# Performance work log

Hardware: AMD Instinct MI355X
Metric: run time of the kernel (lower is better)

Reference implementation:

```python
import math
import jax, jax.numpy as jnp
import numpy as np

D_MODEL, N_HEADS, QKV, D_HEAD, D_FF, N_BLOCKS, IN_DIM = 288, 8, 328, 41, 1315, 4, 83
B, S = 1024, 128
EPS = 1e-5


def setup_inputs() -> dict:
    key = jax.random.key(0)
    ks = iter(jax.random.split(key, 64))
    def rn(shape, scale=0.05):
        return jax.random.normal(next(ks), shape, jnp.float32) * scale
    inp = {
        "x": jax.random.normal(next(ks), (B, S, IN_DIM), jnp.float32),
        "Wp": rn((D_MODEL, IN_DIM)), "bp": rn((D_MODEL,)),
        "phase": rn((D_MODEL,)),
        "Wq": rn((N_BLOCKS, QKV, D_MODEL)), "bq": rn((N_BLOCKS, QKV)),
        "Wk": rn((N_BLOCKS, QKV, D_MODEL)), "bk": rn((N_BLOCKS, QKV)),
        "Wv": rn((N_BLOCKS, QKV, D_MODEL)), "bv": rn((N_BLOCKS, QKV)),
        "Wo": rn((N_BLOCKS, D_MODEL, QKV)), "bo": rn((N_BLOCKS, D_MODEL)),
        "temp": jnp.ones((N_BLOCKS,), jnp.float32) + rn((N_BLOCKS,), 0.01),
        "qscale": jnp.ones((N_BLOCKS, N_HEADS), jnp.float32) + rn((N_BLOCKS, N_HEADS), 0.01),
        "Wf1": rn((N_BLOCKS, D_FF, D_MODEL)), "bf1": rn((N_BLOCKS, D_FF)),
        "Wf2": rn((N_BLOCKS, D_MODEL, D_FF)), "bf2": rn((N_BLOCKS, D_MODEL)),
        "n1w": jnp.ones((N_BLOCKS, D_MODEL), jnp.float32), "n1b": jnp.zeros((N_BLOCKS, D_MODEL), jnp.float32),
        "n2w": jnp.ones((N_BLOCKS, D_MODEL), jnp.float32), "n2b": jnp.zeros((N_BLOCKS, D_MODEL), jnp.float32),
        "skip": jnp.ones((N_BLOCKS,), jnp.float32),
        "bn_w": jnp.ones((D_MODEL,), jnp.float32), "bn_b": jnp.zeros((D_MODEL,), jnp.float32),
        "bn_mean": rn((D_MODEL,)), "bn_var": jax.random.uniform(next(ks), (D_MODEL,), jnp.float32, 0.5, 1.5),
        "h1w": rn((144, D_MODEL)), "h1b": rn((144,)),
        "h2w": rn((72, 144)), "h2b": rn((72,)),
        "h3w": rn((1, 72)), "h3b": rn((1,)),
        "u1w": rn((72, D_MODEL)), "u1b": rn((72,)),
        "u2w": rn((1, 72)), "u2b": rn((1,)),
    }
    return inp


def _layer_norm(x, w, b):
    mu = jnp.mean(x, axis=-1, keepdims=True)
    var = jnp.mean((x - mu) ** 2, axis=-1, keepdims=True)
    return (x - mu) * jax.lax.rsqrt(var + EPS) * w + b


def reference(x, Wp, bp, phase, Wq, bq, Wk, bk, Wv, bv, Wo, bo, temp, qscale,
              Wf1, bf1, Wf2, bf2, n1w, n1b, n2w, n2b, skip,
              bn_w, bn_b, bn_mean, bn_var,
              h1w, h1b, h2w, h2b, h3w, h3b, u1w, u1b, u2w, u2b):
    Bsz, Sl, _ = x.shape
    # input projection
    h = jnp.einsum('bsi,di->bsd', x, Wp) + bp
    # sinusoidal positional encoding modulated by cos(quantum_phase)
    pos = jnp.arange(Sl, dtype=jnp.float32)[:, None]
    div = jnp.exp(jnp.arange(0, D_MODEL, 2, dtype=jnp.float32) * (-math.log(10000.0) / D_MODEL))
    pe = jnp.zeros((Sl, D_MODEL), jnp.float32)
    pe = pe.at[:, 0::2].set(jnp.sin(pos * div)).at[:, 1::2].set(jnp.cos(pos * div))
    h = h + pe * jnp.cos(phase)

    for l in range(N_BLOCKS):
        # attention with temperature-scaled softmax + post-softmax per-head scale
        q = (jnp.einsum('bsd,qd->bsq', h, Wq[l]) + bq[l]).reshape(Bsz, Sl, N_HEADS, D_HEAD)
        k = (jnp.einsum('bsd,qd->bsq', h, Wk[l]) + bk[l]).reshape(Bsz, Sl, N_HEADS, D_HEAD)
        v = (jnp.einsum('bsd,qd->bsq', h, Wv[l]) + bv[l]).reshape(Bsz, Sl, N_HEADS, D_HEAD)
        scale = math.sqrt(D_HEAD) * temp[l]
        scores = jnp.einsum('bqhd,bkhd->bhqk', q, k) / scale  # [B,H,S,S]
        attn = jax.nn.softmax(scores, axis=-1) * qscale[l][None, :, None, None]
        o = jnp.einsum('bhqk,bkhd->bqhd', attn, v).reshape(Bsz, Sl, QKV)
        o = jnp.einsum('bsq,dq->bsd', o, Wo[l]) + bo[l]
        h = _layer_norm(h + skip[l] * o, n1w[l], n1b[l])
        # GELU FFN (exact erf gelu, dropout inactive in eval)
        f = jax.nn.gelu(jnp.einsum('bsd,fd->bsf', h, Wf1[l]) + bf1[l], approximate=False)
        f = jnp.einsum('bsf,df->bsd', f, Wf2[l]) + bf2[l]
        h = _layer_norm(h + f, n2w[l], n2b[l])

    pooled = jnp.mean(h, axis=1)  # [B, D_MODEL]
    # output head: BatchNorm1d (eval, running stats) -> GELU -> MLP
    z = (pooled - bn_mean) * jax.lax.rsqrt(bn_var + EPS) * bn_w + bn_b
    z = jax.nn.gelu(z, approximate=False)
    z = jax.nn.gelu(z @ h1w.T + h1b, approximate=False)
    z = jax.nn.gelu(z @ h2w.T + h2b, approximate=False)
    pred = z @ h3w.T + h3b  # [B, 1]
    # uncertainty head
    u = jax.nn.relu(pooled @ u1w.T + u1b)
    unc = jax.nn.softplus(u @ u2w.T + u2b)  # [B, 1]
    return pred, unc
```

## Files before the change

### kernel.cpp

```cpp
#include <hip/hip_runtime.h>
#include <cstdint>

typedef __attribute__((ext_vector_type(8))) short short8;
typedef __attribute__((ext_vector_type(4))) short s4v;
typedef __attribute__((ext_vector_type(4))) float floatx4;

#define DEV __device__ __forceinline__

DEV short f2bf(float f) {
  unsigned u = __builtin_bit_cast(unsigned, f);
  u += 0x7fffu + ((u >> 16) & 1u);
  return (short)(u >> 16);
}
DEV short f2bf_ru(float f) {
  unsigned u = __builtin_bit_cast(unsigned, f);
  return (short)((u + 0x8000u) >> 16);
}
DEV float bf2f(short s) {
  unsigned u = ((unsigned)(unsigned short)s) << 16;
  return __builtin_bit_cast(float, u);
}
DEV float gelu_exact(float x) {
  return 0.5f * x * (1.0f + erff(x * 0.70710678118654752f));
}
DEV float gelu_fast(float x) {
  const float t2 = 1.5957691216057308f * (x + 0.044715f * x * x * x);
  return x / (1.0f + __expf(-t2));
}
DEV void gload16(const void* g, void* l) {
  __builtin_amdgcn_global_load_lds((const __attribute__((address_space(1))) void*)g,
                                   (__attribute__((address_space(3))) void*)l,
                                   16, 0, 0);
}

template<int MODE>
__global__ __launch_bounds__(256)
void gemm_kernel(const short* __restrict__ A, const short* __restrict__ Bw,
                 const float* __restrict__ bias, short* __restrict__ C,
                 const float* __restrict__ pe,
                 int K, int lda, int ldb, int ldc, int Nstore, int NT, long hstride)
{
  __shared__ __align__(16) short lds[128 * 136];
  short* As = lds;
  short* Bs = lds + 128 * 32;
  short* Ct = lds;

  const int tid  = threadIdx.x;
  const int wave = tid >> 6, lane = tid & 63;
  const int quad = lane >> 4, r16 = lane & 15;
  const int per = gridDim.x >> 3;
  const int gti = (blockIdx.x & 7) * per + (blockIdx.x >> 3);
  const int mt = gti / NT, nt = gti - mt * NT;
  const int wm = (wave >> 1) * 64, wn = (wave & 1) * 64;

  const long Abase = (long)mt * 128 * lda;
  const long Bbase = (long)nt * 128 * ldb;

  const int row0 = tid >> 2,         cc0 = (tid & 3) ^ ((row0 >> 1) & 3);
  const int row1 = (256 + tid) >> 2, cc1 = ((256 + tid) & 3) ^ ((row1 >> 1) & 3);

  floatx4 acc[4][4] = {};

  for (int k0 = 0; k0 < K; k0 += 32) {
    __syncthreads();
    gload16(A  + Abase + (long)row0 * lda + k0 + cc0 * 8, &As[(0 * 256 + wave * 64) * 8]);
    gload16(A  + Abase + (long)row1 * lda + k0 + cc1 * 8, &As[(1 * 256 + wave * 64) * 8]);
    gload16(Bw + Bbase + (long)row0 * ldb + k0 + cc0 * 8, &Bs[(0 * 256 + wave * 64) * 8]);
    gload16(Bw + Bbase + (long)row1 * ldb + k0 + cc1 * 8, &Bs[(1 * 256 + wave * 64) * 8]);
    __syncthreads();

    short8 af[4], bfr[4];
#pragma unroll
    for (int i = 0; i < 4; ++i) {
      const int R = wm + i * 16 + r16;
      af[i] = *(const short8*)&As[R * 32 + (quad ^ ((R >> 1) & 3)) * 8];
    }
#pragma unroll
    for (int j = 0; j < 4; ++j) {
      const int R = wn + j * 16 + r16;
      bfr[j] = *(const short8*)&Bs[R * 32 + (quad ^ ((R >> 1) & 3)) * 8];
    }
#pragma unroll
    for (int i = 0; i < 4; ++i)
#pragma unroll
      for (int j = 0; j < 4; ++j)
        acc[i][j] = __builtin_amdgcn_mfma_f32_16x16x32_bf16(bfr[j], af[i], acc[i][j], 0, 0, 0);
  }

  const int mb0 = mt * 128, tb = nt * 128;

  __syncthreads();
#pragma unroll
  for (int j = 0; j < 4; ++j) {
    const int n0 = wn + j * 16 + quad * 4;
    const floatx4 b4 = *(const floatx4*)&bias[tb + n0];
#pragma unroll
    for (int i = 0; i < 4; ++i) {
      const int m = wm + i * 16 + r16;
      floatx4 v = acc[i][j] + b4;
      if (MODE == 1) {
#pragma unroll
        for (int rg = 0; rg < 4; ++rg) v[rg] = gelu_fast(v[rg]);
      }
      if (MODE == 2) {
        const floatx4 p4 = *(const floatx4*)&pe[((mb0 + m) & 127) * 384 + tb + n0];
        v = v + p4;
      }
      s4v o4;
#pragma unroll
      for (int rg = 0; rg < 4; ++rg) o4[rg] = f2bf_ru(v[rg]);
      *(s4v*)&Ct[m * 136 + n0] = o4;
    }
  }
  __syncthreads();

#pragma unroll
  for (int rr = 0; rr < 8; ++rr) {
    const int chunk = rr * 256 + tid;
    const int row = chunk >> 4, ch = chunk & 15;
    const int gcol = tb + ch * 8;
    if (MODE == 3) {
      const int g = gcol / 48, d0 = gcol - g * 48;
      *(short8*)(C + (long)g * hstride + (long)(mb0 + row) * 48 + d0) =
          *(const short8*)&Ct[row * 136 + ch * 8];
    } else if (gcol < Nstore) {
      *(short8*)(C + (long)(mb0 + row) * ldc + gcol) = *(const short8*)&Ct[row * 136 + ch * 8];
    }
  }
}

template<bool AHEAD>
__global__ __launch_bounds__(512, 4)
void gemm_ln_kernel(const short* __restrict__ A, const short* __restrict__ Bw,
                    const float* __restrict__ bias, short* __restrict__ h,
                    const float* __restrict__ lnw, const float* __restrict__ lnb,
                    const float* __restrict__ skip_p, int layer, int use_skip,
                    int K, int lda, int ldb, long ahs)
{
  __shared__ __align__(16) short lds[128 * 296];
  short* As = lds;
  short* Bs = lds + 128 * 32;
  short* Hs = lds;

  const int tid  = threadIdx.x;
  const int wave = tid >> 6, lane = tid & 63;
  const int quad = lane >> 4, r16 = lane & 15;
  const int mt = blockIdx.x;
  const long mrow0 = (long)mt * 128;

  floatx4 acc[18] = {};

  for (int k0 = 0; k0 < K; k0 += 32) {
    __syncthreads();
    for (int c = tid; c < 1664; c += 512) {
      const void* src;
      if (c < 512) {
        const int row = c >> 2, cc = (c & 3) ^ ((row >> 1) & 3);
        if (AHEAD) {
          const int kc = k0 + cc * 8;
          const int g = kc / 48, d = kc - g * 48;
          src = A + (long)g * ahs + (mrow0 + row) * 48 + d;
        } else {
          src = A + (mrow0 + row) * lda + k0 + cc * 8;
        }
      } else {
        const int cb = c - 512;
        const int row = cb >> 2, cc = (cb & 3) ^ ((row >> 1) & 3);
        src = Bw + (long)row * ldb + k0 + cc * 8;
      }
      gload16(src, &lds[(size_t)(c & ~63) * 8]);
    }
    __syncthreads();

    const int Ra = wave * 16 + r16;
    const short8 af = *(const short8*)&As[Ra * 32 + (quad ^ ((Ra >> 1) & 3)) * 8];
#pragma unroll
    for (int t = 0; t < 18; ++t) {
      const int Rb = t * 16 + r16;
      const short8 bfr = *(const short8*)&Bs[Rb * 32 + (quad ^ ((Rb >> 1) & 3)) * 8];
      acc[t] = __builtin_amdgcn_mfma_f32_16x16x32_bf16(bfr, af, acc[t], 0, 0, 0);
    }
  }

  __syncthreads();
  for (int c = tid; c < 4608; c += 512) {
    const int row = c / 36, ch = c - row * 36;
    *(short8*)&Hs[row * 296 + ch * 8] =
        *(const short8*)(h + (mrow0 + row) * 288 + ch * 8);
  }
  __syncthreads();

  const float skipv = use_skip ? skip_p[layer] : 1.0f;
  const int m = wave * 16 + r16;

  float ps = 0.f, pss = 0.f;
#pragma unroll
  for (int t = 0; t < 18; ++t) {
    const int n0 = t * 16 + quad * 4;
    const floatx4 b4 = *(const floatx4*)&bias[n0];
    const s4v h4 = *(const s4v*)&Hs[m * 296 + n0];
#pragma unroll
    for (int rg = 0; rg < 4; ++rg) {
      const float y = bf2f(h4[rg]) + skipv * (acc[t][rg] + b4[rg]);
      acc[t][rg] = y;
      ps += y; pss += y * y;
    }
  }
  ps  += __shfl_xor(ps, 16);  ps  += __shfl_xor(ps, 32);
  pss += __shfl_xor(pss, 16); pss += __shfl_xor(pss, 32);
  const float mean = ps * (1.f / 288.f);
  const float var  = pss * (1.f / 288.f) - mean * mean;
  const float rstd = rsqrtf(var + 1e-5f);

#pragma unroll
  for (int t = 0; t < 18; ++t) {
    const int n0 = t * 16 + quad * 4;
    const floatx4 w4 = *(const floatx4*)&lnw[n0];
    const floatx4 l4 = *(const floatx4*)&lnb[n0];
    s4v o4;
#pragma unroll
    for (int rg = 0; rg < 4; ++rg)
      o4[rg] = f2bf_ru((acc[t][rg] - mean) * rstd * w4[rg] + l4[rg]);
    *(s4v*)&Hs[m * 296 + n0] = o4;
  }
  __syncthreads();

  for (int c = tid; c < 4608; c += 512) {
    const int row = c / 36, ch = c - row * 36;
    *(short8*)(h + (mrow0 + row) * 288 + ch * 8) =
        *(const short8*)&Hs[row * 296 + ch * 8];
  }
}

__global__ __launch_bounds__(256)
void attn_kernel(short* __restrict__ qkv,
                 const float* __restrict__ qscale, int layer, long Mc)
{
  __shared__ __align__(16) short qk[2 * 128 * 72];
  __shared__ __align__(16) short vsT[48 * 136 + 32];
  __shared__ float red[2][2][64];

  short* qs = qk;
  short* ks = qk + 128 * 72;
  short* Pb = qk;

  const int b = blockIdx.x, h = blockIdx.y;
  const int tid = threadIdx.x;
  const long sec = Mc * 48;
  const short* qg = qkv + (long)h * sec + (long)b * 128 * 48;
  const short* kg = qg + 8 * sec;
  const short* vg = qg + 16 * sec;
  short* og = qkv + (long)(16 + h) * sec + (long)b * 128 * 48;

  for (int c = tid; c < 768; c += 256) {
    const int s = c / 6, dc = c - (c / 6) * 6;
    *(short8*)&qs[s * 72 + dc * 8] = *(const short8*)(qg + (long)s * 48 + dc * 8);
    *(short8*)&ks[s * 72 + dc * 8] = *(const short8*)(kg + (long)s * 48 + dc * 8);
  }
  {
    short8 z;
#pragma unroll
    for (int j = 0; j < 8; ++j) z[j] = 0;
    for (int c = tid; c < 384; c += 256) {
      const int s = c / 3, t = c - (c / 3) * 3;
      *(short8*)&qs[s * 72 + 48 + t * 8] = z;
      *(short8*)&ks[s * 72 + 48 + t * 8] = z;
    }
  }
  for (int c = tid; c < 768; c += 256) {
    const int s = c & 127, dc = c >> 7;
    const short8 tv = *(const short8*)(vg + (long)s * 48 + dc * 8);
#pragma unroll
    for (int j = 0; j < 8; ++j) {
      const int row = dc * 8 + j;
      vsT[row * 136 + ((row >> 3) & 3) * 8 + s] = tv[j];
    }
  }
  __syncthreads();

  const int wave = tid >> 6, lane = tid & 63;
  const int quad = lane >> 4, r16 = lane & 15;
  const int wm = (wave >> 1) * 64, wn = (wave & 1) * 64;
  const int rh = wave >> 1, ch = wave & 1;
  const float qsc = qscale[layer * 8 + h];

  floatx4 acc[4][4] = {};
#pragma unroll
  for (int kk = 0; kk < 2; ++kk) {
    const int k0 = kk * 32;
    short8 af[4], bfr[4];
#pragma unroll
    for (int i = 0; i < 4; ++i)
      af[i] = *(const short8*)&qs[(wm + i * 16 + r16) * 72 + k0 + quad * 8];
#pragma unroll
    for (int j = 0; j < 4; ++j)
      bfr[j] = *(const short8*)&ks[(wn + j * 16 + r16) * 72 + k0 + quad * 8];
#pragma unroll
    for (int i = 0; i < 4; ++i)
#pragma unroll
      for (int j = 0; j < 4; ++j)
        acc[i][j] = __builtin_amdgcn_mfma_f32_16x16x32_bf16(bfr[j], af[i], acc[i][j], 0, 0, 0);
  }

  float rmax[4], rsum[4];
#pragma unroll
  for (int i = 0; i < 4; ++i) {
    float m = acc[i][0][0];
#pragma unroll
    for (int j = 0; j < 4; ++j)
#pragma unroll
      for (int rg = 0; rg < 4; ++rg) m = fmaxf(m, acc[i][j][rg]);
    m = fmaxf(m, __shfl_xor(m, 16));
    m = fmaxf(m, __shfl_xor(m, 32));
    rmax[i] = m;
  }
  if (lane < 16)
#pragma unroll
    for (int i = 0; i < 4; ++i) red[rh][ch][i * 16 + r16] = rmax[i];
  __syncthreads();
#pragma unroll
  for (int i = 0; i < 4; ++i)
    rmax[i] = fmaxf(red[rh][0][i * 16 + r16], red[rh][1][i * 16 + r16]);

#pragma unroll
  for (int i = 0; i < 4; ++i) {
    float s = 0.f;
#pragma unroll
    for (int j = 0; j < 4; ++j)
#pragma unroll
      for (int rg = 0; rg < 4; ++rg) {
        const float e = __expf(acc[i][j][rg] - rmax[i]);
        acc[i][j][rg] = e;
        s += e;
      }
    s += __shfl_xor(s, 16);
    s += __shfl_xor(s, 32);
    rsum[i] = s;
  }
  __syncthreads();
  if (lane < 16)
#pragma unroll
    for (int i = 0; i < 4; ++i) red[rh][ch][i * 16 + r16] = rsum[i];
  __syncthreads();
#pragma unroll
  for (int i = 0; i < 4; ++i)
    rmax[i] = qsc / (red[rh][0][i * 16 + r16] + red[rh][1][i * 16 + r16]);

#pragma unroll
  for (int i = 0; i < 4; ++i) {
    const int sq = wm + i * 16 + r16;
#pragma unroll
    for (int j = 0; j < 4; ++j) {
      const int sk0 = wn + j * 16 + quad * 4;
      s4v p4;
#pragma unroll
      for (int rg = 0; rg < 4; ++rg) p4[rg] = f2bf_ru(acc[i][j][rg] * rmax[i]);
      *(s4v*)&Pb[sq * 136 + sk0] = p4;
    }
  }
  __syncthreads();

  const int om = (wave >> 1) * 64, on = (wave & 1) * 32;
  const int jn = (on == 0) ? 2 : 1;
  floatx4 oacc[4][2] = {};
  for (int kk = 0; kk < 4; ++kk) {
    const int k0 = kk * 32;
    short8 af[4], bfr[2];
#pragma unroll
    for (int i = 0; i < 4; ++i)
      af[i] = *(const short8*)&Pb[(om + i * 16 + r16) * 136 + k0 + quad * 8];
    for (int j = 0; j < jn; ++j) {
      const int row = on + j * 16 + r16;
      bfr[j] = *(const short8*)&vsT[row * 136 + ((row >> 3) & 3) * 8 + k0 + quad * 8];
    }
#pragma unroll
    for (int i = 0; i < 4; ++i)
      for (int j = 0; j < jn; ++j)
        oacc[i][j] = __builtin_amdgcn_mfma_f32_16x16x32_bf16(bfr[j], af[i], oacc[i][j], 0, 0, 0);
  }
#pragma unroll
  for (int i = 0; i < 4; ++i)
    for (int j = 0; j < jn; ++j) {
      const int d0 = on + j * 16 + quad * 4;
      const int sq = om + i * 16 + r16;
      s4v o4;
#pragma unroll
      for (int rg = 0; rg < 4; ++rg) o4[rg] = f2bf_ru(oacc[i][j][rg]);
      *(s4v*)(og + (long)sq * 48 + d0) = o4;
    }
}

__global__ __launch_bounds__(256)
void head_kernel(const short* __restrict__ hb, float* __restrict__ out,
                 const float* bn_w, const float* bn_b, const float* bn_mean, const float* bn_var,
                 const float* h1w, const float* h1b, const float* h2w, const float* h2b,
                 const float* h3w, const float* h3b,
                 const float* u1w, const float* u1b, const float* u2w, const float* u2b)
{
  __shared__ float psum[252][8];
  __shared__ float pooled[288], z[288], z1[144], z2[72], uu[72];
  const int b = blockIdx.x, tid = threadIdx.x;

  if (tid < 252) {
    const int cch = tid % 36, grp = tid / 36;
    float a[8];
#pragma unroll
    for (int j = 0; j < 8; ++j) a[j] = 0.f;
    for (int r = grp; r < 128; r += 7) {
      const short8 hv = *(const short8*)(hb + ((long)b * 128 + r) * 288 + cch * 8);
#pragma unroll
      for (int j = 0; j < 8; ++j) a[j] += bf2f(hv[j]);
    }
#pragma unroll
    for (int j = 0; j < 8; ++j) psum[tid][j] = a[j];
  }
  __syncthreads();
  for (int d = tid; d < 288; d += 256) {
    const int cch = d >> 3, j = d & 7;
    float s = 0.f;
#pragma unroll
    for (int g = 0; g < 7; ++g) s += psum[g * 36 + cch][j];
    pooled[d] = s * (1.f / 128.f);
  }
  __syncthreads();

  for (int d = tid; d < 288; d += 256) {
    const float p = pooled[d];
    z[d] = gelu_exact((p - bn_mean[d]) * rsqrtf(bn_var[d] + 1e-5f) * bn_w[d] + bn_b[d]);
  }
  __syncthreads();

  if (tid < 144) {
    float s = h1b[tid];
    for (int k = 0; k < 288; ++k) s += z[k] * h1w[tid * 288 + k];
    z1[tid] = gelu_exact(s);
  } else if (tid < 216) {
    const int t = tid - 144;
    float s = u1b[t];
    for (int k = 0; k < 288; ++k) s += pooled[k] * u1w[t * 288 + k];
    uu[t] = fmaxf(s, 0.f);
  }
  __syncthreads();

  if (tid < 72) {
    float s = h2b[tid];
    for (int k = 0; k < 144; ++k) s += z1[k] * h2w[tid * 144 + k];
    z2[tid] = gelu_exact(s);
  }
  __syncthreads();

  if (tid == 0) {
    float s = h3b[0];
    for (int k = 0; k < 72; ++k) s += z2[k] * h3w[k];
    out[b] = s;
  }
  if (tid == 64) {
    float s = u2b[0];
    for (int k = 0; k < 72; ++k) s += uu[k] * u2w[k];
    out[1024 + b] = (s > 20.f) ? s : log1pf(__expf(s));
  }
}

__global__ void conv_w_kernel(const float* __restrict__ src, short* __restrict__ dst,
                              int N, int K, int Npad, int Kpad, int total)
{
  const int i = blockIdx.x * 256 + threadIdx.x;
  if (i >= total) return;
  const int kk = i % Kpad;
  const int t  = i / Kpad;
  const int n  = t % Npad;
  const int l  = t / Npad;
  const float v = (n < N && kk < K) ? src[((long)l * N + n) * K + kk] : 0.f;
  dst[i] = f2bf(v);
}

__global__ void conv_b_kernel(const float* __restrict__ src, float* __restrict__ dst,
                              int N, int Npad, int total)
{
  const int i = blockIdx.x * 256 + threadIdx.x;
  if (i >= total) return;
  const int n = i % Npad, l = i / Npad;
  dst[i] = (n < N) ? src[l * N + n] : 0.f;
}

__global__ void conv_wqkv_kernel(const float* __restrict__ Wq, const float* __restrict__ Wk,
                                 const float* __restrict__ Wv, const float* __restrict__ temp,
                                 short* __restrict__ dst)
{
  const int i = blockIdx.x * 256 + threadIdx.x;
  if (i >= 4 * 1152 * 288) return;
  const int kk = i % 288;
  const int t  = i / 288;
  const int r  = t % 1152;
  const int l  = t / 1152;
  const int g  = r / 48, d = r - (r / 48) * 48;
  const int sec = g >> 3, head = g & 7;
  float v = 0.f;
  if (d < 41) {
    const float* W = (sec == 0) ? Wq : (sec == 1) ? Wk : Wv;
    v = W[((long)l * 328 + head * 41 + d) * 288 + kk];
    if (sec == 0) v *= 1.0f / (6.4031242374328485f * temp[l]);
  }
  dst[i] = f2bf(v);
}

__global__ void conv_bqkv_kernel(const float* __restrict__ bq, const float* __restrict__ bk,
                                 const float* __restrict__ bv, const float* __restrict__ temp,
                                 float* __restrict__ dst)
{
  const int i = blockIdx.x * 256 + threadIdx.x;
  if (i >= 4 * 1152) return;
  const int r = i % 1152, l = i / 1152;
  const int g = r / 48, d = r - (r / 48) * 48;
  const int sec = g >> 3, head = g & 7;
  float v = 0.f;
  if (d < 41) {
    const float* b = (sec == 0) ? bq : (sec == 1) ? bk : bv;
    v = b[l * 328 + head * 41 + d];
    if (sec == 0) v *= 1.0f / (6.4031242374328485f * temp[l]);
  }
  dst[i] = v;
}

__global__ void conv_wo_kernel(const float* __restrict__ Wo, short* __restrict__ dst)
{
  const int i = blockIdx.x * 256 + threadIdx.x;
  if (i >= 4 * 288 * 384) return;
  const int kk = i % 384;
  const int t  = i / 384;
  const int n  = t % 288;
  const int l  = t / 288;
  const int head = kk / 48, d = kk - head * 48;
  float v = 0.f;
  if (d < 41) v = Wo[((long)l * 288 + n) * 328 + head * 41 + d];
  dst[i] = f2bf(v);
}

__global__ void conv_x_kernel(const float* __restrict__ x, short* __restrict__ xb, int total)
{
  const int i = blockIdx.x * 256 + threadIdx.x;
  if (i >= total) return;
  const int c = i % 96;
  const int r = i / 96;
  xb[i] = f2bf((c < 83) ? x[(long)r * 83 + c] : 0.f);
}

__global__ void pe_kernel(const float* __restrict__ phase, float* __restrict__ pe_mod)
{
  const int i = blockIdx.x * 256 + threadIdx.x;
  if (i >= 128 * 384) return;
  const int d = i % 384, s = i / 384;
  float out = 0.f;
  if (d < 288) {
    const int pair = d >> 1;
    const float divv = expf((float)(2 * pair) * (-9.210340371976184f / 288.f));
    const float arg = (float)s * divv;
    const float v = (d & 1) ? cosf(arg) : sinf(arg);
    out = v * cosf(phase[d]);
  }
  pe_mod[i] = out;
}

extern "C" void kernel_launch(void* const* d_in, const int* in_sizes, int n_in,
                              void* d_out, int out_size, void* d_ws, size_t ws_size,
                              hipStream_t stream)
{
  (void)in_sizes; (void)n_in; (void)out_size;

  const float* x     = (const float*)d_in[0];
  const float* Wp    = (const float*)d_in[1];
  const float* bp    = (const float*)d_in[2];
  const float* phase = (const float*)d_in[3];
  const float* Wq    = (const float*)d_in[4];
  const float* bq    = (const float*)d_in[5];
  const float* Wk    = (const float*)d_in[6];
  const float* bk    = (const float*)d_in[7];
  const float* Wv    = (const float*)d_in[8];
  const float* bv    = (const float*)d_in[9];
  const float* Wo    = (const float*)d_in[10];
  const float* bo    = (const float*)d_in[11];
  const float* temp  = (const float*)d_in[12];
  const float* qscale= (const float*)d_in[13];
  const float* Wf1   = (const float*)d_in[14];
  const float* bf1   = (const float*)d_in[15];
  const float* Wf2   = (const float*)d_in[16];
  const float* bf2   = (const float*)d_in[17];
  const float* n1w   = (const float*)d_in[18];
  const float* n1b   = (const float*)d_in[19];
  const float* n2w   = (const float*)d_in[20];
  const float* n2b   = (const float*)d_in[21];
  const float* skip  = (const float*)d_in[22];
  const float* bn_w  = (const float*)d_in[23];
  const float* bn_b  = (const float*)d_in[24];
  const float* bn_mean=(const float*)d_in[25];
  const float* bn_var= (const float*)d_in[26];
  const float* h1w   = (const float*)d_in[27];
  const float* h1b   = (const float*)d_in[28];
  const float* h2w   = (const float*)d_in[29];
  const float* h2b   = (const float*)d_in[30];
  const float* h3w   = (const float*)d_in[31];
  const float* h3b   = (const float*)d_in[32];
  const float* u1w   = (const float*)d_in[33];
  const float* u1b   = (const float*)d_in[34];
  const float* u2w   = (const float*)d_in[35];
  const float* u2b   = (const float*)d_in[36];

  char* ws = (char*)d_ws;
  size_t off = 0;
  auto alloc = [&](size_t n) -> char* {
    off = (off + 255) & ~(size_t)255;
    char* p = ws + off;
    off += n;
    return p;
  };

  const long M = 131072;

  short* h_bf   = (short*)alloc((size_t)M * 288 * 2);
  float* pe_mod = (float*)alloc(128 * 384 * 4);

  short* Wp_b   = (short*)alloc((size_t)384 * 96 * 2);
  short* Wqkv_b = (short*)alloc((size_t)4 * 1152 * 288 * 2);
  short* Wo_b   = (short*)alloc((size_t)4 * 288 * 384 * 2);
  short* Wf1_b  = (short*)alloc((size_t)4 * 1408 * 288 * 2);
  short* Wf2_b  = (short*)alloc((size_t)4 * 384 * 1344 * 2);

  float* bp_p   = (float*)alloc((size_t)384 * 4);
  float* bqkv_p = (float*)alloc((size_t)4 * 1152 * 4);
  float* bo_p   = (float*)alloc((size_t)4 * 384 * 4);
  float* bf1_p  = (float*)alloc((size_t)4 * 1408 * 4);
  float* bf2_p  = (float*)alloc((size_t)4 * 384 * 4);

  const size_t fixed = off;
  int NC = 1;
  while (NC < 16 && fixed + (size_t)(M / NC) * 2304 + (1u << 20) > ws_size) NC <<= 1;
  const long Mc = M / NC;
  const long Mc2 = Mc / 2;
  const long sec = Mc * 48;

  char* R = alloc((size_t)Mc * 2304);
  short* qkv_bf = (short*)R;
  short* f_bf   = (short*)R;
  short* x_bfc  = (short*)R;

  const dim3 blk(256);

  auto conv_w = [&](const float* s, short* d, int N, int K, int Np, int Kp, int L) {
    const int total = L * Np * Kp;
    conv_w_kernel<<<dim3((total + 255) / 256), blk, 0, stream>>>(s, d, N, K, Np, Kp, total);
  };
  auto conv_b = [&](const float* s, float* d, int N, int Np, int L) {
    const int total = L * Np;
    conv_b_kernel<<<dim3((total + 255) / 256), blk, 0, stream>>>(s, d, N, Np, total);
  };
  conv_w(Wp,  Wp_b,  288,   83, 384,   96, 1);
  conv_wqkv_kernel<<<dim3((4 * 1152 * 288 + 255) / 256), blk, 0, stream>>>(Wq, Wk, Wv, temp, Wqkv_b);
  conv_wo_kernel<<<dim3((4 * 288 * 384 + 255) / 256), blk, 0, stream>>>(Wo, Wo_b);
  conv_w(Wf1, Wf1_b, 1315, 288, 1408, 288, 4);
  conv_w(Wf2, Wf2_b, 288, 1315, 384, 1344, 4);
  conv_b(bp,  bp_p,  288,  384, 1);
  conv_bqkv_kernel<<<dim3((4 * 1152 + 255) / 256), blk, 0, stream>>>(bq, bk, bv, temp, bqkv_p);
  conv_b(bo,  bo_p,  288,  384, 4);
  conv_b(bf1, bf1_p, 1315, 1408, 4);
  conv_b(bf2, bf2_p, 288,  384, 4);
  pe_kernel<<<dim3((128 * 384 + 255) / 256), blk, 0, stream>>>(phase, pe_mod);

  auto gemm = [&](int mode, const short* A, const short* Bmat, const float* bias,
                  short* C, const float* pe, int K, int lda, int ldb, int ldc,
                  int Nstore, int NT, long Mrows, long hstride) {
    const dim3 grid((unsigned)((Mrows / 128) * NT));
    switch (mode) {
      case 0: gemm_kernel<0><<<grid, blk, 0, stream>>>(A, Bmat, bias, C, pe, K, lda, ldb, ldc, Nstore, NT, hstride); break;
      case 1: gemm_kernel<1><<<grid, blk, 0, stream>>>(A, Bmat, bias, C, pe, K, lda, ldb, ldc, Nstore, NT, hstride); break;
      case 2: gemm_kernel<2><<<grid, blk, 0, stream>>>(A, Bmat, bias, C, pe, K, lda, ldb, ldc, Nstore, NT, hstride); break;
      default: gemm_kernel<3><<<grid, blk, 0, stream>>>(A, Bmat, bias, C, pe, K, lda, ldb, ldc, Nstore, NT, hstride); break;
    }
  };

  for (int c = 0; c < NC; ++c) {
    const float* x_c = x + (size_t)c * Mc * 83;
    short* h_c = h_bf + (size_t)c * Mc * 288;

    const int xtot = (int)(Mc * 96);
    conv_x_kernel<<<dim3((xtot + 255) / 256), blk, 0, stream>>>(x_c, x_bfc, xtot);

    gemm(2, x_bfc, Wp_b, bp_p, h_c, pe_mod, 96, 96, 96, 288, 288, 3, Mc, 0);

    for (int l = 0; l < 4; ++l) {
      const short* Wqkv_l = Wqkv_b + (size_t)l * 1152 * 288;
      const short* Wo_l   = Wo_b   + (size_t)l * 288 * 384;
      const short* Wf1_l  = Wf1_b  + (size_t)l * 1408 * 288;
      const short* Wf2_l  = Wf2_b  + (size_t)l * 384 * 1344;

      gemm(3, h_c, Wqkv_l, bqkv_p + l * 1152, qkv_bf, nullptr,
           288, 288, 288, 0, 1152, 9, Mc, sec);

      attn_kernel<<<dim3((unsigned)(Mc / 128), 8), blk, 0, stream>>>(
          qkv_bf, qscale, l, Mc);

      gemm_ln_kernel<true><<<dim3((unsigned)(Mc / 128)), dim3(512), 0, stream>>>(
          qkv_bf + 16 * sec, Wo_l, bo_p + l * 384, h_c, n1w + l * 288, n1b + l * 288,
          skip, l, 1, 384, 48, 384, sec);

      for (int s = 0; s < 2; ++s) {
        short* h_s = h_c + (size_t)s * Mc2 * 288;
        gemm(1, h_s, Wf1_l, bf1_p + l * 1408, f_bf, nullptr,
             288, 288, 288, 1344, 1344, 11, Mc2, 0);
        gemm_ln_kernel<false><<<dim3((unsigned)(Mc2 / 128)), dim3(512), 0, stream>>>(
            f_bf, Wf2_l, bf2_p + l * 384, h_s, n2w + l * 288, n2b + l * 288,
            skip, l, 0, 1344, 1344, 1344, 0);
      }
    }
  }

  head_kernel<<<dim3(1024), blk, 0, stream>>>(h_bf, (float*)d_out,
      bn_w, bn_b, bn_mean, bn_var,
      h1w, h1b, h2w, h2b, h3w, h3b,
      u1w, u1b, u2w, u2b);
}
```

Baseline: 3.710 ms.

## Double-buffer LDS staging in GEMM kernels and retile GEMM+LayerNorm waves to 2x2

Both the plain GEMM and the fused GEMM+LayerNorm kernels now use two LDS buffers, issuing global-to-LDS loads for the next K slice before computing on the current one, with one barrier per iteration instead of two. The GEMM+LN kernel also changes its wave layout from 8x1 (16 rows by all 288 cols) to 4x2 (32 rows by 144 cols), so each B fragment feeds two MFMAs. Row statistics are then combined across the two column waves through a small shared-memory reduction with an extra barrier. The intent is to hide load latency and cut LDS B-fragment reads, at the cost of more LDS use (which may limit occupancy) and the extra reduction step.

```diff
diff --git a/kernel.cpp b/kernel.cpp
--- a/kernel.cpp
+++ b/kernel.cpp
@@ -41,8 +41,6 @@
                  int K, int lda, int ldb, int ldc, int Nstore, int NT, long hstride)
 {
   __shared__ __align__(16) short lds[128 * 136];
-  short* As = lds;
-  short* Bs = lds + 128 * 32;
   short* Ct = lds;
 
   const int tid  = threadIdx.x;
@@ -61,35 +59,54 @@
 
   floatx4 acc[4][4] = {};
 
-  for (int k0 = 0; k0 < K; k0 += 32) {
-    __syncthreads();
-    gload16(A  + Abase + (long)row0 * lda + k0 + cc0 * 8, &As[(0 * 256 + wave * 64) * 8]);
-    gload16(A  + Abase + (long)row1 * lda + k0 + cc1 * 8, &As[(1 * 256 + wave * 64) * 8]);
-    gload16(Bw + Bbase + (long)row0 * ldb + k0 + cc0 * 8, &Bs[(0 * 256 + wave * 64) * 8]);
-    gload16(Bw + Bbase + (long)row1 * ldb + k0 + cc1 * 8, &Bs[(1 * 256 + wave * 64) * 8]);
-    __syncthreads();
-
+  auto stage = [&](short* As_, short* Bs_, int k0) {
+    gload16(A  + Abase + (long)row0 * lda + k0 + cc0 * 8, &As_[(wave * 64) * 8]);
+    gload16(A  + Abase + (long)row1 * lda + k0 + cc1 * 8, &As_[(256 + wave * 64) * 8]);
+    gload16(Bw + Bbase + (long)row0 * ldb + k0 + cc0 * 8, &Bs_[(wave * 64) * 8]);
+    gload16(Bw + Bbase + (long)row1 * ldb + k0 + cc1 * 8, &Bs_[(256 + wave * 64) * 8]);
+  };
+  auto compute = [&](const short* As_, const short* Bs_) {
     short8 af[4], bfr[4];
 #pragma unroll
     for (int i = 0; i < 4; ++i) {
       const int R = wm + i * 16 + r16;
-      af[i] = *(const short8*)&As[R * 32 + (quad ^ ((R >> 1) & 3)) * 8];
+      af[i] = *(const short8*)&As_[R * 32 + (quad ^ ((R >> 1) & 3)) * 8];
     }
 #pragma unroll
     for (int j = 0; j < 4; ++j) {
       const int R = wn + j * 16 + r16;
-      bfr[j] = *(const short8*)&Bs[R * 32 + (quad ^ ((R >> 1) & 3)) * 8];
+      bfr[j] = *(const short8*)&Bs_[R * 32 + (quad ^ ((R >> 1) & 3)) * 8];
     }
 #pragma unroll
     for (int i = 0; i < 4; ++i)
 #pragma unroll
       for (int j = 0; j < 4; ++j)
         acc[i][j] = __builtin_amdgcn_mfma_f32_16x16x32_bf16(bfr[j], af[i], acc[i][j], 0, 0, 0);
+  };
+
+  short* const A0  = lds;
+  short* const Bb0 = lds + 4096;
+  short* const A1  = lds + 8192;
+  short* const Bb1 = lds + 12288;
+
+  stage(A0, Bb0, 0);
+  __syncthreads();
+  int k0 = 0;
+  while (true) {
+    if (k0 + 32 < K) stage(A1, Bb1, k0 + 32);
+    compute(A0, Bb0);
+    __syncthreads();
+    k0 += 32;
+    if (k0 >= K) break;
+    if (k0 + 32 < K) stage(A0, Bb0, k0 + 32);
+    compute(A1, Bb1);
+    __syncthreads();
+    k0 += 32;
+    if (k0 >= K) break;
   }
 
   const int mb0 = mt * 128, tb = nt * 128;
 
-  __syncthreads();
 #pragma unroll
   for (int j = 0; j < 4; ++j) {
     const int n0 = wn + j * 16 + quad * 4;
@@ -138,20 +155,20 @@
                     int K, int lda, int ldb, long ahs)
 {
   __shared__ __align__(16) short lds[128 * 296];
-  short* As = lds;
-  short* Bs = lds + 128 * 32;
+  __shared__ float redp[4][2][2][16];
+  __shared__ float reds[4][2][2][16];
   short* Hs = lds;
 
   const int tid  = threadIdx.x;
   const int wave = tid >> 6, lane = tid & 63;
   const int quad = lane >> 4, r16 = lane & 15;
+  const int wr = wave >> 1, wc = wave & 1;
   const int mt = blockIdx.x;
   const long mrow0 = (long)mt * 128;
 
-  floatx4 acc[18] = {};
-
-  for (int k0 = 0; k0 < K; k0 += 32) {
-    __syncthreads();
+  floatx4 acc[2][9] = {};
+
+  auto stage = [&](short* buf, int k0) {
     for (int c = tid; c < 1664; c += 512) {
       const void* src;
       if (c < 512) {
@@ -168,21 +185,44 @@
         const int row = cb >> 2, cc = (cb & 3) ^ ((row >> 1) & 3);
         src = Bw + (long)row * ldb + k0 + cc * 8;
       }
-      gload16(src, &lds[(size_t)(c & ~63) * 8]);
-    }
+      gload16(src, &buf[(size_t)(c & ~63) * 8]);
+    }
+  };
+
+  auto compute = [&](const short* buf) {
+    const short* As_ = buf;
+    const short* Bs_ = buf + 4096;
+    const int Ra0 = wr * 32 + r16, Ra1 = Ra0 + 16;
+    const short8 af0 = *(const short8*)&As_[Ra0 * 32 + (quad ^ ((Ra0 >> 1) & 3)) * 8];
+    const short8 af1 = *(const short8*)&As_[Ra1 * 32 + (quad ^ ((Ra1 >> 1) & 3)) * 8];
+#pragma unroll
+    for (int t = 0; t < 9; ++t) {
+      const int Rb = wc * 144 + t * 16 + r16;
+      const short8 b = *(const short8*)&Bs_[Rb * 32 + (quad ^ ((Rb >> 1) & 3)) * 8];
+      acc[0][t] = __builtin_amdgcn_mfma_f32_16x16x32_bf16(b, af0, acc[0][t], 0, 0, 0);
+      acc[1][t] = __builtin_amdgcn_mfma_f32_16x16x32_bf16(b, af1, acc[1][t], 0, 0, 0);
+    }
+  };
+
+  short* const B0 = lds;
+  short* const B1 = lds + 13312;
+
+  stage(B0, 0);
+  __syncthreads();
+  int k0 = 0;
+  while (true) {
+    if (k0 + 32 < K) stage(B1, k0 + 32);
+    compute(B0);
     __syncthreads();
-
-    const int Ra = wave * 16 + r16;
-    const short8 af = *(const short8*)&As[Ra * 32 + (quad ^ ((Ra >> 1) & 3)) * 8];
-#pragma unroll
-    for (int t = 0; t < 18; ++t) {
-      const int Rb = t * 16 + r16;
-      const short8 bfr = *(const short8*)&Bs[Rb * 32 + (quad ^ ((Rb >> 1) & 3)) * 8];
-      acc[t] = __builtin_amdgcn_mfma_f32_16x16x32_bf16(bfr, af, acc[t], 0, 0, 0);
-    }
-  }
-
-  __syncthreads();
+    k0 += 32;
+    if (k0 >= K) break;
+    if (k0 + 32 < K) stage(B0, k0 + 32);
+    compute(B1);
+    __syncthreads();
+    k0 += 32;
+    if (k0 >= K) break;
+  }
+
   for (int c = tid; c < 4608; c += 512) {
     const int row = c / 36, ch = c - row * 36;
     *(short8*)&Hs[row * 296 + ch * 8] =
@@ -191,37 +231,54 @@
   __syncthreads();
 
   const float skipv = use_skip ? skip_p[layer] : 1.0f;
-  const int m = wave * 16 + r16;
-
-  float ps = 0.f, pss = 0.f;
-#pragma unroll
-  for (int t = 0; t < 18; ++t) {
-    const int n0 = t * 16 + quad * 4;
+  const int m0 = wr * 32 + r16, m1 = m0 + 16;
+
+  float ps0 = 0.f, ss0 = 0.f, ps1 = 0.f, ss1 = 0.f;
+#pragma unroll
+  for (int t = 0; t < 9; ++t) {
+    const int n0 = wc * 144 + t * 16 + quad * 4;
     const floatx4 b4 = *(const floatx4*)&bias[n0];
-    const s4v h4 = *(const s4v*)&Hs[m * 296 + n0];
+    const s4v h40 = *(const s4v*)&Hs[m0 * 296 + n0];
+    const s4v h41 = *(const s4v*)&Hs[m1 * 296 + n0];
 #pragma unroll
     for (int rg = 0; rg < 4; ++rg) {
-      const float y = bf2f(h4[rg]) + skipv * (acc[t][rg] + b4[rg]);
-      acc[t][rg] = y;
-      ps += y; pss += y * y;
-    }
-  }
-  ps  += __shfl_xor(ps, 16);  ps  += __shfl_xor(ps, 32);
-  pss += __shfl_xor(pss, 16); pss += __shfl_xor(pss, 32);
-  const float mean = ps * (1.f / 288.f);
-  const float var  = pss * (1.f / 288.f) - mean * mean;
-  const float rstd = rsqrtf(var + 1e-5f);
-
-#pragma unroll
-  for (int t = 0; t < 18; ++t) {
-    const int n0 = t * 16 + quad * 4;
+      const float y0 = bf2f(h40[rg]) + skipv * (acc[0][t][rg] + b4[rg]);
+      const float y1 = bf2f(h41[rg]) + skipv * (acc[1][t][rg] + b4[rg]);
+      acc[0][t][rg] = y0; acc[1][t][rg] = y1;
+      ps0 += y0; ss0 += y0 * y0;
+      ps1 += y1; ss1 += y1 * y1;
+    }
+  }
+  ps0 += __shfl_xor(ps0, 16); ps0 += __shfl_xor(ps0, 32);
+  ss0 += __shfl_xor(ss0, 16); ss0 += __shfl_xor(ss0, 32);
+  ps1 += __shfl_xor(ps1, 16); ps1 += __shfl_xor(ps1, 32);
+  ss1 += __shfl_xor(ss1, 16); ss1 += __shfl_xor(ss1, 32);
+  if (lane < 16) {
+    redp[wr][wc][0][r16] = ps0; redp[wr][wc][1][r16] = ps1;
+    reds[wr][wc][0][r16] = ss0; reds[wr][wc][1][r16] = ss1;
+  }
+  __syncthreads();
+  const float psum0 = redp[wr][0][0][r16] + redp[wr][1][0][r16];
+  const float psum1 = redp[wr][0][1][r16] + redp[wr][1][1][r16];
+  const float ssum0 = reds[wr][0][0][r16] + reds[wr][1][0][r16];
+  const float ssum1 = reds[wr][0][1][r16] + reds[wr][1][1][r16];
+  const float mean0 = psum0 * (1.f / 288.f), mean1 = psum1 * (1.f / 288.f);
+  const float rstd0 = rsqrtf(ssum0 * (1.f / 288.f) - mean0 * mean0 + 1e-5f);
+  const float rstd1 = rsqrtf(ssum1 * (1.f / 288.f) - mean1 * mean1 + 1e-5f);
+
+#pragma unroll
+  for (int t = 0; t < 9; ++t) {
+    const int n0 = wc * 144 + t * 16 + quad * 4;
     const floatx4 w4 = *(const floatx4*)&lnw[n0];
     const floatx4 l4 = *(const floatx4*)&lnb[n0];
-    s4v o4;
-#pragma unroll
-    for (int rg = 0; rg < 4; ++rg)
-      o4[rg] = f2bf_ru((acc[t][rg] - mean) * rstd * w4[rg] + l4[rg]);
-    *(s4v*)&Hs[m * 296 + n0] = o4;
+    s4v o0, o1;
+#pragma unroll
+    for (int rg = 0; rg < 4; ++rg) {
+      o0[rg] = f2bf_ru((acc[0][t][rg] - mean0) * rstd0 * w4[rg] + l4[rg]);
+      o1[rg] = f2bf_ru((acc[1][t][rg] - mean1) * rstd1 * w4[rg] + l4[rg]);
+    }
+    *(s4v*)&Hs[m0 * 296 + n0] = o0;
+    *(s4v*)&Hs[m1 * 296 + n0] = o1;
   }
   __syncthreads();
 
```

Measured after the change: 3.673 ms. No clear change (-1.0%).
